# Kernel optimization log

Measured on AMD Instinct MI355X. Metric: run time of the kernel, lower is better.

## Reference

```python
import jax, jax.numpy as jnp
import numpy as np

B, H, S, D = 4, 16, 4096, 64

def _phi(x):
    # feature map for linear attention: elu(x) + 1 (positive features)
    return jax.nn.elu(x) + 1.0

def setup_inputs() -> dict:
    key = jax.random.key(0)
    kq, kk, kv = jax.random.split(key, 3)
    return {
        "query": jax.random.normal(kq, (B, H, S, D), dtype=jnp.float32),
        "key": jax.random.normal(kk, (B, H, S, D), dtype=jnp.float32),
        "value": jax.random.normal(kv, (B, H, S, D), dtype=jnp.float32),
        "attention_mask": jnp.ones((B, S), dtype=jnp.float32),
    }

def reference(query, key, value, attention_mask):
    head_dim = query.shape[-1]
    scale = 1.0 / jnp.sqrt(jnp.sqrt(jnp.float32(head_dim)))
    q = query * scale
    k = key * scale
    phi_q = _phi(q)
    phi_k = _phi(k)
    m = attention_mask[:, None, :, None]  # [B,1,S,1]
    phi_q = phi_q * m
    phi_k = phi_k * m
    # kv_term: [B,H,D,Dv]
    kv_term = jnp.einsum("bhsd,bhse->bhde", phi_k, value)
    out = jnp.einsum("bhsd,bhde->bhse", phi_q, kv_term)
    # normalizer: phi_q @ sum_s phi_k -> [B,H,S,1]
    k_one = jnp.sum(phi_k, axis=-2)  # [B,H,D]
    normalizer = jnp.einsum("bhsd,bhd->bhs", phi_q, k_one)[..., None]
    return out / (normalizer + 1e-8)
```

## Files before the change

### kernel.cpp

```cpp
#include <hip/hip_runtime.h>

#define BDIM 4
#define HDIM 16
#define SDIM 4096
#define DDIM 64
#define NBH (BDIM * HDIM)

#define P1_TS 16
#define P1_NCHUNK 16
#define P1_CHUNK (SDIM / P1_NCHUNK)

#define P2_MT 64

__device__ __forceinline__ float phi_f(float x) {
    return x > 0.0f ? x + 1.0f : __expf(x);
}

__global__ __launch_bounds__(256) void la_phase1(
    const float* __restrict__ K, const float* __restrict__ V,
    const float* __restrict__ mask,
    float* __restrict__ kv, float* __restrict__ kone)
{
    __shared__ float kT[P1_TS][DDIM];
    __shared__ float vT[P1_TS][DDIM];

    const int bh = blockIdx.y;
    const int b  = bh / HDIM;
    const int t  = threadIdx.x;
    const int row = t >> 4;
    const int c4  = (t & 15) << 2;
    const int d0  = (t >> 4) << 2;
    const int e0  = (t & 15) << 2;
    const int s_base = blockIdx.x * P1_CHUNK;

    const float* Kb = K + (size_t)bh * SDIM * DDIM;
    const float* Vb = V + (size_t)bh * SDIM * DDIM;
    const float* mb = mask + (size_t)b * SDIM;

    const float scale = 0.35355339059327373f;

    float acc[4][4] = {};
    float k1[4] = {0.f, 0.f, 0.f, 0.f};

    int s0 = s_base + row;
    float4 kf = *(const float4*)(Kb + (size_t)s0 * DDIM + c4);
    float4 vf = *(const float4*)(Vb + (size_t)s0 * DDIM + c4);
    float  m  = mb[s0];

    for (int st = 0; st < P1_CHUNK; st += P1_TS) {
        const float p0 = phi_f(kf.x * scale) * m;
        const float p1 = phi_f(kf.y * scale) * m;
        const float p2 = phi_f(kf.z * scale) * m;
        const float p3 = phi_f(kf.w * scale) * m;
        __syncthreads();
        kT[row][c4 + 0] = p0;
        kT[row][c4 + 1] = p1;
        kT[row][c4 + 2] = p2;
        kT[row][c4 + 3] = p3;
        *(float4*)&vT[row][c4] = vf;
        __syncthreads();

        k1[0] += p0; k1[1] += p1; k1[2] += p2; k1[3] += p3;

        if (st + P1_TS < P1_CHUNK) {
            const int sn = s_base + st + P1_TS + row;
            kf = *(const float4*)(Kb + (size_t)sn * DDIM + c4);
            vf = *(const float4*)(Vb + (size_t)sn * DDIM + c4);
            m  = mb[sn];
        }

        #pragma unroll
        for (int ss = 0; ss < P1_TS; ++ss) {
            const float4 a  = *(const float4*)&kT[ss][d0];
            const float4 v4 = *(const float4*)&vT[ss][e0];
            acc[0][0] += a.x * v4.x; acc[0][1] += a.x * v4.y; acc[0][2] += a.x * v4.z; acc[0][3] += a.x * v4.w;
            acc[1][0] += a.y * v4.x; acc[1][1] += a.y * v4.y; acc[1][2] += a.y * v4.z; acc[1][3] += a.y * v4.w;
            acc[2][0] += a.z * v4.x; acc[2][1] += a.z * v4.y; acc[2][2] += a.z * v4.z; acc[2][3] += a.z * v4.w;
            acc[3][0] += a.w * v4.x; acc[3][1] += a.w * v4.y; acc[3][2] += a.w * v4.z; acc[3][3] += a.w * v4.w;
        }
    }

    float* kvb = kv + (size_t)bh * DDIM * DDIM;
    #pragma unroll
    for (int i = 0; i < 4; ++i)
        #pragma unroll
        for (int j = 0; j < 4; ++j)
            atomicAdd(&kvb[(d0 + i) * DDIM + e0 + j], acc[i][j]);

    __syncthreads();
    kT[row][c4 + 0] = k1[0];
    kT[row][c4 + 1] = k1[1];
    kT[row][c4 + 2] = k1[2];
    kT[row][c4 + 3] = k1[3];
    __syncthreads();
    if (t < DDIM) {
        float s1 = 0.f;
        #pragma unroll
        for (int r = 0; r < P1_TS; ++r) s1 += kT[r][t];
        atomicAdd(&kone[bh * DDIM + t], s1);
    }
}

__global__ __launch_bounds__(256) void la_phase2(
    const float* __restrict__ Q, const float* __restrict__ mask,
    const float* __restrict__ kv, const float* __restrict__ kone,
    float* __restrict__ out)
{
    __shared__ float kvL[DDIM][DDIM];
    __shared__ float pqT[DDIM][P2_MT + 4];
    __shared__ float koL[DDIM];

    const int bh = blockIdx.y;
    const int b  = bh / HDIM;
    const int t  = threadIdx.x;
    const int s_base = blockIdx.x * P2_MT;

    const float scale = 0.35355339059327373f;

    {
        const float4* src = (const float4*)(kv + (size_t)bh * DDIM * DDIM);
        float4* dst = (float4*)&kvL[0][0];
        #pragma unroll
        for (int i = 0; i < 4; ++i) dst[t + 256 * i] = src[t + 256 * i];
        if (t < DDIM) koL[t] = kone[bh * DDIM + t];
    }
    {
        const float* Qb = Q + (size_t)bh * SDIM * DDIM;
        const float* mb = mask + (size_t)b * SDIM;
        const int lr = t & 15;
        const int c4 = (t >> 4) << 2;
        #pragma unroll
        for (int k = 0; k < 4; ++k) {
            const int r = lr + 16 * k;
            const int s = s_base + r;
            const float4 qf = *(const float4*)(Qb + (size_t)s * DDIM + c4);
            const float mm = mb[s];
            pqT[c4 + 0][r] = phi_f(qf.x * scale) * mm;
            pqT[c4 + 1][r] = phi_f(qf.y * scale) * mm;
            pqT[c4 + 2][r] = phi_f(qf.z * scale) * mm;
            pqT[c4 + 3][r] = phi_f(qf.w * scale) * mm;
        }
    }
    __syncthreads();

    const int r0 = (t >> 4) << 2;
    const int e0 = (t & 15) << 2;
    float acc[4][4] = {};
    float nrm[4] = {0.f, 0.f, 0.f, 0.f};

    #pragma unroll 16
    for (int d = 0; d < DDIM; ++d) {
        const float4 a  = *(const float4*)&pqT[d][r0];
        const float4 bb = *(const float4*)&kvL[d][e0];
        const float ko = koL[d];
        acc[0][0] += a.x * bb.x; acc[0][1] += a.x * bb.y; acc[0][2] += a.x * bb.z; acc[0][3] += a.x * bb.w;
        acc[1][0] += a.y * bb.x; acc[1][1] += a.y * bb.y; acc[1][2] += a.y * bb.z; acc[1][3] += a.y * bb.w;
        acc[2][0] += a.z * bb.x; acc[2][1] += a.z * bb.y; acc[2][2] += a.z * bb.z; acc[2][3] += a.z * bb.w;
        acc[3][0] += a.w * bb.x; acc[3][1] += a.w * bb.y; acc[3][2] += a.w * bb.z; acc[3][3] += a.w * bb.w;
        nrm[0] += a.x * ko; nrm[1] += a.y * ko; nrm[2] += a.z * ko; nrm[3] += a.w * ko;
    }

    float* ob = out + ((size_t)bh * SDIM + s_base) * DDIM;
    #pragma unroll
    for (int i = 0; i < 4; ++i) {
        const float inv = 1.0f / (nrm[i] + 1e-8f);
        float4 o;
        o.x = acc[i][0] * inv;
        o.y = acc[i][1] * inv;
        o.z = acc[i][2] * inv;
        o.w = acc[i][3] * inv;
        *(float4*)(ob + (size_t)(r0 + i) * DDIM + e0) = o;
    }
}

extern "C" void kernel_launch(void* const* d_in, const int* in_sizes, int n_in,
                              void* d_out, int out_size, void* d_ws, size_t ws_size,
                              hipStream_t stream) {
    const float* Q = (const float*)d_in[0];
    const float* K = (const float*)d_in[1];
    const float* V = (const float*)d_in[2];
    const float* M = (const float*)d_in[3];
    float* out  = (float*)d_out;
    float* kv   = (float*)d_ws;
    float* kone = kv + (size_t)NBH * DDIM * DDIM;

    const size_t zero_bytes =
        ((size_t)NBH * DDIM * DDIM + (size_t)NBH * DDIM) * sizeof(float);
    hipMemsetAsync(d_ws, 0, zero_bytes, stream);

    dim3 g1(P1_NCHUNK, NBH);
    la_phase1<<<g1, dim3(256), 0, stream>>>(K, V, M, kv, kone);

    dim3 g2(SDIM / P2_MT, NBH);
    la_phase2<<<g2, dim3(256), 0, stream>>>(Q, M, kv, kone, out);
}
```

Measured before the change: 278.5 us.

## Replace atomics with per-chunk partials plus reduce, double-buffer phase1, widen phase2 tiles

Phase 1 now writes each sequence chunk's partial KV and k-sum to a separate workspace slot, and a new reduce kernel sums them, removing the memset and the global atomics. It also uses up to 32 chunks when the workspace allows, for more parallelism. Phase 1 double-buffers its shared tiles so each iteration needs only one barrier. Phase 2 processes 128 rows per block with 512 threads, which halves the number of KV reloads. The cost is an extra kernel launch, more workspace, and larger phase-2 blocks that may lower occupancy.

```diff
diff --git a/kernel.cpp b/kernel.cpp
--- a/kernel.cpp
+++ b/kernel.cpp
@@ -7,31 +7,30 @@
 #define NBH (BDIM * HDIM)
 
 #define P1_TS 16
-#define P1_NCHUNK 16
-#define P1_CHUNK (SDIM / P1_NCHUNK)
-
-#define P2_MT 64
+#define BH_STRIDE (DDIM * DDIM + DDIM)
+#define CHUNK_FLOATS (NBH * BH_STRIDE)
+#define P2_MT 128
 
 __device__ __forceinline__ float phi_f(float x) {
     return x > 0.0f ? x + 1.0f : __expf(x);
 }
 
+template<bool ATOMIC>
 __global__ __launch_bounds__(256) void la_phase1(
     const float* __restrict__ K, const float* __restrict__ V,
-    const float* __restrict__ mask,
-    float* __restrict__ kv, float* __restrict__ kone)
+    const float* __restrict__ mask, float* __restrict__ outp, int chunk_rows)
 {
-    __shared__ float kT[P1_TS][DDIM];
-    __shared__ float vT[P1_TS][DDIM];
-
-    const int bh = blockIdx.y;
-    const int b  = bh / HDIM;
-    const int t  = threadIdx.x;
+    __shared__ float kT[2][P1_TS][DDIM];
+    __shared__ float vT[2][P1_TS][DDIM];
+
+    const int bh  = blockIdx.y;
+    const int b   = bh / HDIM;
+    const int t   = threadIdx.x;
     const int row = t >> 4;
     const int c4  = (t & 15) << 2;
-    const int d0  = (t >> 4) << 2;
-    const int e0  = (t & 15) << 2;
-    const int s_base = blockIdx.x * P1_CHUNK;
+    const int d0  = row << 2;
+    const int e0  = c4;
+    const int s_base = blockIdx.x * chunk_rows;
 
     const float* Kb = K + (size_t)bh * SDIM * DDIM;
     const float* Vb = V + (size_t)bh * SDIM * DDIM;
@@ -47,23 +46,23 @@
     float4 vf = *(const float4*)(Vb + (size_t)s0 * DDIM + c4);
     float  m  = mb[s0];
 
-    for (int st = 0; st < P1_CHUNK; st += P1_TS) {
+    const int ntiles = chunk_rows >> 4;
+    int p = 0;
+    for (int tt = 0; tt < ntiles; ++tt) {
         const float p0 = phi_f(kf.x * scale) * m;
         const float p1 = phi_f(kf.y * scale) * m;
         const float p2 = phi_f(kf.z * scale) * m;
         const float p3 = phi_f(kf.w * scale) * m;
+        kT[p][row][c4 + 0] = p0;
+        kT[p][row][c4 + 1] = p1;
+        kT[p][row][c4 + 2] = p2;
+        kT[p][row][c4 + 3] = p3;
+        *(float4*)&vT[p][row][c4] = vf;
+        k1[0] += p0; k1[1] += p1; k1[2] += p2; k1[3] += p3;
         __syncthreads();
-        kT[row][c4 + 0] = p0;
-        kT[row][c4 + 1] = p1;
-        kT[row][c4 + 2] = p2;
-        kT[row][c4 + 3] = p3;
-        *(float4*)&vT[row][c4] = vf;
-        __syncthreads();
-
-        k1[0] += p0; k1[1] += p1; k1[2] += p2; k1[3] += p3;
-
-        if (st + P1_TS < P1_CHUNK) {
-            const int sn = s_base + st + P1_TS + row;
+
+        if (tt + 1 < ntiles) {
+            const int sn = s_base + ((tt + 1) << 4) + row;
             kf = *(const float4*)(Kb + (size_t)sn * DDIM + c4);
             vf = *(const float4*)(Vb + (size_t)sn * DDIM + c4);
             m  = mb[sn];
@@ -71,40 +70,62 @@
 
         #pragma unroll
         for (int ss = 0; ss < P1_TS; ++ss) {
-            const float4 a  = *(const float4*)&kT[ss][d0];
-            const float4 v4 = *(const float4*)&vT[ss][e0];
+            const float4 a  = *(const float4*)&kT[p][ss][d0];
+            const float4 v4 = *(const float4*)&vT[p][ss][e0];
             acc[0][0] += a.x * v4.x; acc[0][1] += a.x * v4.y; acc[0][2] += a.x * v4.z; acc[0][3] += a.x * v4.w;
             acc[1][0] += a.y * v4.x; acc[1][1] += a.y * v4.y; acc[1][2] += a.y * v4.z; acc[1][3] += a.y * v4.w;
             acc[2][0] += a.z * v4.x; acc[2][1] += a.z * v4.y; acc[2][2] += a.z * v4.z; acc[2][3] += a.z * v4.w;
             acc[3][0] += a.w * v4.x; acc[3][1] += a.w * v4.y; acc[3][2] += a.w * v4.z; acc[3][3] += a.w * v4.w;
         }
-    }
-
-    float* kvb = kv + (size_t)bh * DDIM * DDIM;
-    #pragma unroll
-    for (int i = 0; i < 4; ++i)
-        #pragma unroll
-        for (int j = 0; j < 4; ++j)
-            atomicAdd(&kvb[(d0 + i) * DDIM + e0 + j], acc[i][j]);
+        p ^= 1;
+    }
+
+    float* base = ATOMIC ? (outp + (size_t)bh * BH_STRIDE)
+                         : (outp + ((size_t)blockIdx.x * NBH + bh) * BH_STRIDE);
+    if (ATOMIC) {
+        #pragma unroll
+        for (int i = 0; i < 4; ++i)
+            #pragma unroll
+            for (int j = 0; j < 4; ++j)
+                atomicAdd(&base[(d0 + i) * DDIM + e0 + j], acc[i][j]);
+    } else {
+        #pragma unroll
+        for (int i = 0; i < 4; ++i)
+            *(float4*)&base[(d0 + i) * DDIM + e0] =
+                make_float4(acc[i][0], acc[i][1], acc[i][2], acc[i][3]);
+    }
 
     __syncthreads();
-    kT[row][c4 + 0] = k1[0];
-    kT[row][c4 + 1] = k1[1];
-    kT[row][c4 + 2] = k1[2];
-    kT[row][c4 + 3] = k1[3];
+    kT[0][row][c4 + 0] = k1[0];
+    kT[0][row][c4 + 1] = k1[1];
+    kT[0][row][c4 + 2] = k1[2];
+    kT[0][row][c4 + 3] = k1[3];
     __syncthreads();
     if (t < DDIM) {
         float s1 = 0.f;
         #pragma unroll
-        for (int r = 0; r < P1_TS; ++r) s1 += kT[r][t];
-        atomicAdd(&kone[bh * DDIM + t], s1);
-    }
-}
-
-__global__ __launch_bounds__(256) void la_phase2(
+        for (int r = 0; r < P1_TS; ++r) s1 += kT[0][r][t];
+        if (ATOMIC) atomicAdd(&base[DDIM * DDIM + t], s1);
+        else        base[DDIM * DDIM + t] = s1;
+    }
+}
+
+__global__ __launch_bounds__(256) void la_reduce(
+    const float* __restrict__ part, float* __restrict__ fin, int nc)
+{
+    const int g = blockIdx.x * 256 + threadIdx.x;
+    const float4* p4 = (const float4*)part;
+    float4 s = p4[g];
+    for (int c = 1; c < nc; ++c) {
+        const float4 v = p4[(size_t)c * (CHUNK_FLOATS / 4) + g];
+        s.x += v.x; s.y += v.y; s.z += v.z; s.w += v.w;
+    }
+    ((float4*)fin)[g] = s;
+}
+
+__global__ __launch_bounds__(512) void la_phase2(
     const float* __restrict__ Q, const float* __restrict__ mask,
-    const float* __restrict__ kv, const float* __restrict__ kone,
-    float* __restrict__ out)
+    const float* __restrict__ fin_all, float* __restrict__ out)
 {
     __shared__ float kvL[DDIM][DDIM];
     __shared__ float pqT[DDIM][P2_MT + 4];
@@ -116,22 +137,24 @@
     const int s_base = blockIdx.x * P2_MT;
 
     const float scale = 0.35355339059327373f;
+    const float* fin = fin_all + (size_t)bh * BH_STRIDE;
 
     {
-        const float4* src = (const float4*)(kv + (size_t)bh * DDIM * DDIM);
+        const float4* src = (const float4*)fin;
         float4* dst = (float4*)&kvL[0][0];
-        #pragma unroll
-        for (int i = 0; i < 4; ++i) dst[t + 256 * i] = src[t + 256 * i];
-        if (t < DDIM) koL[t] = kone[bh * DDIM + t];
+        dst[t] = src[t];
+        dst[t + 512] = src[t + 512];
+        if (t < DDIM) koL[t] = fin[DDIM * DDIM + t];
     }
     {
         const float* Qb = Q + (size_t)bh * SDIM * DDIM;
         const float* mb = mask + (size_t)b * SDIM;
-        const int lr = t & 15;
-        const int c4 = (t >> 4) << 2;
+        const int lr   = t & 15;
+        const int c4   = ((t >> 4) & 15) << 2;
+        const int half = t >> 8;
         #pragma unroll
         for (int k = 0; k < 4; ++k) {
-            const int r = lr + 16 * k;
+            const int r = lr + 16 * (half * 4 + k);
             const int s = s_base + r;
             const float4 qf = *(const float4*)(Qb + (size_t)s * DDIM + c4);
             const float mm = mb[s];
@@ -180,17 +203,24 @@
     const float* K = (const float*)d_in[1];
     const float* V = (const float*)d_in[2];
     const float* M = (const float*)d_in[3];
-    float* out  = (float*)d_out;
-    float* kv   = (float*)d_ws;
-    float* kone = kv + (size_t)NBH * DDIM * DDIM;
-
-    const size_t zero_bytes =
-        ((size_t)NBH * DDIM * DDIM + (size_t)NBH * DDIM) * sizeof(float);
-    hipMemsetAsync(d_ws, 0, zero_bytes, stream);
-
-    dim3 g1(P1_NCHUNK, NBH);
-    la_phase1<<<g1, dim3(256), 0, stream>>>(K, V, M, kv, kone);
-
-    dim3 g2(SDIM / P2_MT, NBH);
-    la_phase2<<<g2, dim3(256), 0, stream>>>(Q, M, kv, kone, out);
-}
+    float* out = (float*)d_out;
+
+    const size_t chunk_bytes = (size_t)CHUNK_FLOATS * sizeof(float);
+
+    int nc = 0;
+    if      (ws_size >= 33 * chunk_bytes) nc = 32;
+    else if (ws_size >= 17 * chunk_bytes) nc = 16;
+
+    if (nc > 0) {
+        float* part = (float*)d_ws;
+        float* fin  = part + (size_t)nc * CHUNK_FLOATS;
+        la_phase1<false><<<dim3(nc, NBH), dim3(256), 0, stream>>>(K, V, M, part, SDIM / nc);
+        la_reduce<<<dim3(CHUNK_FLOATS / 4 / 256), dim3(256), 0, stream>>>(part, fin, nc);
+        la_phase2<<<dim3(SDIM / P2_MT, NBH), dim3(512), 0, stream>>>(Q, M, fin, out);
+    } else {
+        float* fin = (float*)d_ws;
+        hipMemsetAsync(d_ws, 0, chunk_bytes, stream);
+        la_phase1<true><<<dim3(16, NBH), dim3(256), 0, stream>>>(K, V, M, fin, SDIM / 16);
+        la_phase2<<<dim3(SDIM / P2_MT, NBH), dim3(512), 0, stream>>>(Q, M, fin, out);
+    }
+}
```

Result: faster. 248.0 us (-11.0%).
